# Optimization experiments

Hardware: AMD Instinct MI355X
Metric: run time of the kernel (lower is better)

## Reference

```python
import jax, jax.numpy as jnp
import numpy as np

N = 8192          # num nodes
E = 262144        # num edges
F_IN = 512        # dataset.num_features
HID = 256         # hidden_dim
C = 16            # dataset.num_classes
ALPHA = 1.0
GAMMA = 1.0
EPS = 0.4
LN_EPS = 1e-5


def setup_inputs() -> dict:
    key = jax.random.key(0)
    ks = jax.random.split(key, 16)
    x = jax.random.normal(ks[0], (N, F_IN), dtype=jnp.float32)
    edge_index = jax.random.randint(ks[1], (2, E), 0, N, dtype=jnp.int64)
    def lin(k, fan_in, fan_out):
        s = 1.0 / np.sqrt(fan_in)
        return jax.random.uniform(k, (fan_in, fan_out), jnp.float32, -s, s)
    return {
        "x": x,
        "edge_index": edge_index,
        "W0": lin(ks[2], F_IN, HID), "b0": jnp.zeros((HID,), jnp.float32),
        "ln0_g": jnp.ones((HID,), jnp.float32), "ln0_b": jnp.zeros((HID,), jnp.float32),
        "W1": lin(ks[3], HID, HID), "b1": jnp.zeros((HID,), jnp.float32),
        "ln1_g": jnp.ones((HID,), jnp.float32), "ln1_b": jnp.zeros((HID,), jnp.float32),
        "W2": lin(ks[4], HID, C), "b2": jnp.zeros((C,), jnp.float32),
    }


def _layernorm(h, g, b):
    mu = jnp.mean(h, axis=-1, keepdims=True)
    var = jnp.var(h, axis=-1, keepdims=True)
    return (h - mu) * jax.lax.rsqrt(var + LN_EPS) * g + b


def _hpf_weight_matrix(edge_index, n, dtype):
    # to_dense_adj with parallel-edge accumulation
    A = jnp.zeros((n, n), dtype).at[edge_index[0], edge_index[1]].add(jnp.asarray(1.0, dtype))
    eye = jnp.eye(n, dtype=dtype)
    A = GAMMA * A + ALPHA * eye
    # D^{-1/2} A D^{-1/2} as fused row/col scaling (same math as the two diag matmuls)
    dinv = jax.lax.rsqrt(jnp.sum(A, axis=1))
    A_hat = dinv[:, None] * A * dinv[None, :]
    # (eps - 1) I + (I - A_hat) == eps*I - A_hat ; keep only positive entries (edge extraction)
    U = EPS * eye - A_hat
    return jnp.where(U > 0, U, jnp.asarray(0.0, dtype))


def reference(x, edge_index, W0, b0, ln0_g, ln0_b, W1, b1, ln1_g, ln1_b, W2, b2):
    Wmat = _hpf_weight_matrix(edge_index, x.shape[0], x.dtype)
    # GCNConv(normalize=False): h' = scatter_{src->tgt}(w * (h@W)[src]) + bias == Wmat^T @ (h@W) + b
    def gcn(h, W, b):
        return Wmat.T @ (h @ W) + b
    h = gcn(x, W0, b0)
    h = _layernorm(jax.nn.relu(h), ln0_g, ln0_b)   # dropout p=0.0 -> identity
    h = gcn(h, W1, b1)
    h = _layernorm(jax.nn.relu(h), ln1_g, ln1_b)
    embedding = gcn(h, W2, b2)
    return embedding, jax.nn.log_softmax(embedding, axis=1)
```

## Files before the change

### kernel.cpp

```cpp
#include <hip/hip_runtime.h>

#define NN 8192
#define NE 262144
#define FIN 512
#define HIDN 256
#define NC 16

typedef __attribute__((ext_vector_type(8))) short bf16x8;
typedef __attribute__((ext_vector_type(4))) short bf16x4;
typedef __attribute__((ext_vector_type(4))) float f32x4;

static __device__ __forceinline__ unsigned short f2bf(float f) {
    union { float f; unsigned u; } v; v.f = f;
    unsigned r = v.u + 0x7FFFu + ((v.u >> 16) & 1u);
    return (unsigned short)(r >> 16);
}

template<int K, int N>
static __device__ __forceinline__ void pack_w(const float* __restrict__ W,
                                              unsigned short* __restrict__ Wp, int f) {
    constexpr int KC = K / 32;
    int lane = f & 63;
    int g = f >> 6;
    int kc = g % KC;
    int nt = g / KC;
    int n = nt * 16 + (lane & 15);
    int kbase = kc * 32 + (lane >> 4) * 8;
    bf16x8 v;
#pragma unroll
    for (int j = 0; j < 8; ++j) v[j] = (short)f2bf(W[(kbase + j) * N + n]);
    *(bf16x8*)&Wp[f * 8] = v;
}

__global__ __launch_bounds__(512) void work_kernel(
    const int* __restrict__ ei,
    const float* __restrict__ W0, const float* __restrict__ W1, const float* __restrict__ W2,
    int* __restrict__ cnt,
    unsigned short* __restrict__ Wp0, unsigned short* __restrict__ Wp1,
    unsigned short* __restrict__ Wp2)
{
    const int tid = threadIdx.x, bid = blockIdx.x;
    if (bid < 207) {
        const int p = bid * 512 + tid;
#pragma unroll
        for (int i = 0; i < 2; ++i) {
            int c = p + i * 105984;
            if (c < NE / 2) {
                int2 s2 = *(const int2*)&ei[c * 2];
                int2 t2 = *(const int2*)&ei[NE + c * 2];
                atomicAdd(&cnt[s2.x], 1);
                atomicAdd(&cnt[s2.y], 1);
                if (s2.x == t2.x) atomicAdd(&cnt[NN + s2.x], 1);
                if (s2.y == t2.y) atomicAdd(&cnt[NN + s2.y], 1);
            }
        }
    } else {
        int gp = (bid - 207) * 512 + tid;
        if (gp < 16384)       pack_w<512, 256>(W0, Wp0, gp);
        else if (gp < 24576)  pack_w<256, 256>(W1, Wp1, gp - 16384);
        else                  pack_w<256, 16 >(W2, Wp2, gp - 24576);
    }
}

static __device__ __forceinline__ void ln_epilogue(
    const f32x4 acc[2], const float* __restrict__ bias, const float* __restrict__ gam,
    const float* __restrict__ bet, const float wdr[4],
    int w, int quad, int l16,
    unsigned short* sH, float red[][16])
{
    float bv[2], gv[2], btv[2];
#pragma unroll
    for (int nt = 0; nt < 2; ++nt) {
        int col = w * 32 + nt * 16 + l16;
        bv[nt] = bias[col]; gv[nt] = gam[col]; btv[nt] = bet[col];
    }
    float vv[2][4], s[4], ss[4];
#pragma unroll
    for (int reg = 0; reg < 4; ++reg) {
        float ps = 0.f, pss = 0.f;
#pragma unroll
        for (int nt = 0; nt < 2; ++nt) {
            float v = fmaxf(fmaf(wdr[reg], acc[nt][reg], bv[nt]), 0.f);
            vv[nt][reg] = v;
            ps += v; pss += v * v;
        }
        s[reg] = ps; ss[reg] = pss;
    }
#pragma unroll
    for (int off = 1; off < 16; off <<= 1)
#pragma unroll
        for (int reg = 0; reg < 4; ++reg) {
            s[reg]  += __shfl_xor(s[reg],  off, 64);
            ss[reg] += __shfl_xor(ss[reg], off, 64);
        }
    __syncthreads();
    if (l16 == 0) {
#pragma unroll
        for (int reg = 0; reg < 4; ++reg) {
            int rl = quad * 4 + reg;
            red[rl][w * 2]     = s[reg];
            red[rl][w * 2 + 1] = ss[reg];
        }
    }
    __syncthreads();
#pragma unroll
    for (int reg = 0; reg < 4; ++reg) {
        int rl = quad * 4 + reg;
        float ts = 0.f, tss = 0.f;
#pragma unroll
        for (int i = 0; i < 8; ++i) { ts += red[rl][2 * i]; tss += red[rl][2 * i + 1]; }
        float mu  = ts * (1.0f / 256.0f);
        float var = tss * (1.0f / 256.0f) - mu * mu;
        float rs  = rsqrtf(var + 1e-5f);
#pragma unroll
        for (int nt = 0; nt < 2; ++nt) {
            float o = (vv[nt][reg] - mu) * rs * gv[nt] + btv[nt];
            sH[rl * 264 + w * 32 + nt * 16 + l16] = f2bf(o);
        }
    }
    __syncthreads();
}

__global__ __launch_bounds__(512) void mega_kernel(
    const float* __restrict__ x,
    const unsigned short* __restrict__ Wp0, const unsigned short* __restrict__ Wp1,
    const unsigned short* __restrict__ Wp2,
    const float* __restrict__ b0, const float* __restrict__ g0, const float* __restrict__ be0,
    const float* __restrict__ b1, const float* __restrict__ g1, const float* __restrict__ be1,
    const float* __restrict__ b2, const int* __restrict__ cnt,
    float* __restrict__ out)
{
    __shared__ unsigned short sX[16 * 520];
    __shared__ unsigned short sH[16 * 264];
    __shared__ float red[16][16];
    __shared__ float swd[16];

    const int tid  = threadIdx.x;
    const int lane = tid & 63, w = tid >> 6;
    const int quad = lane >> 4, l16 = lane & 15;
    const int row0 = blockIdx.x * 16;

    const float4* x4 = (const float4*)x;
    const int idx0 = tid * 2;
    float4 v0 = x4[row0 * 128 + idx0];
    float4 v1 = x4[row0 * 128 + idx0 + 1];
    float4 v2 = x4[row0 * 128 + 1024 + idx0];
    float4 v3 = x4[row0 * 128 + 1024 + idx0 + 1];

    if (tid < 16) {
        int base = cnt[2 * NN];
        int d  = cnt[row0 + tid]      - base;
        int sl = cnt[NN + row0 + tid] - base;
        float u = 0.4f - (1.0f + (float)sl) / (1.0f + (float)d);
        swd[tid] = u > 0.0f ? u : 0.0f;
    }

    {
        int r = idx0 >> 7, c4 = idx0 & 127;
        bf16x8 h;
        h[0] = (short)f2bf(v0.x); h[1] = (short)f2bf(v0.y);
        h[2] = (short)f2bf(v0.z); h[3] = (short)f2bf(v0.w);
        h[4] = (short)f2bf(v1.x); h[5] = (short)f2bf(v1.y);
        h[6] = (short)f2bf(v1.z); h[7] = (short)f2bf(v1.w);
        *(bf16x8*)&sX[r * 520 + c4 * 4] = h;
        int idx1 = idx0 + 1024;
        r = idx1 >> 7; c4 = idx1 & 127;
        h[0] = (short)f2bf(v2.x); h[1] = (short)f2bf(v2.y);
        h[2] = (short)f2bf(v2.z); h[3] = (short)f2bf(v2.w);
        h[4] = (short)f2bf(v3.x); h[5] = (short)f2bf(v3.y);
        h[6] = (short)f2bf(v3.z); h[7] = (short)f2bf(v3.w);
        *(bf16x8*)&sX[r * 520 + c4 * 4] = h;
    }
    __syncthreads();

    float wdr[4];
#pragma unroll
    for (int reg = 0; reg < 4; ++reg) wdr[reg] = swd[quad * 4 + reg];

    const bf16x8* Wp0v = (const bf16x8*)Wp0;
    const bf16x8* Wp1v = (const bf16x8*)Wp1;
    const bf16x8* Wp2v = (const bf16x8*)Wp2;

    f32x4 acc[2];
#pragma unroll
    for (int nt = 0; nt < 2; ++nt) acc[nt] = (f32x4){0.f, 0.f, 0.f, 0.f};
#pragma unroll
    for (int kc = 0; kc < 16; ++kc) {
        bf16x8 a = *(const bf16x8*)&sX[l16 * 520 + kc * 32 + quad * 8];
#pragma unroll
        for (int nt = 0; nt < 2; ++nt) {
            bf16x8 b = Wp0v[((w * 2 + nt) * 16 + kc) * 64 + lane];
            acc[nt] = __builtin_amdgcn_mfma_f32_16x16x32_bf16(a, b, acc[nt], 0, 0, 0);
        }
    }
    ln_epilogue(acc, b0, g0, be0, wdr, w, quad, l16, sH, red);

    f32x4 acc1[2];
#pragma unroll
    for (int nt = 0; nt < 2; ++nt) acc1[nt] = (f32x4){0.f, 0.f, 0.f, 0.f};
#pragma unroll
    for (int kc = 0; kc < 8; ++kc) {
        bf16x8 a = *(const bf16x8*)&sH[l16 * 264 + kc * 32 + quad * 8];
#pragma unroll
        for (int nt = 0; nt < 2; ++nt) {
            bf16x8 b = Wp1v[((w * 2 + nt) * 8 + kc) * 64 + lane];
            acc1[nt] = __builtin_amdgcn_mfma_f32_16x16x32_bf16(a, b, acc1[nt], 0, 0, 0);
        }
    }
    ln_epilogue(acc1, b1, g1, be1, wdr, w, quad, l16, sH, red);

    if (w == 0) {
        f32x4 acch = (f32x4){0.f, 0.f, 0.f, 0.f};
#pragma unroll
        for (int kc = 0; kc < 8; ++kc) {
            bf16x8 a = *(const bf16x8*)&sH[l16 * 264 + kc * 32 + quad * 8];
            bf16x8 b = Wp2v[kc * 64 + lane];
            acch = __builtin_amdgcn_mfma_f32_16x16x32_bf16(a, b, acch, 0, 0, 0);
        }
        float bb = b2[l16];
#pragma unroll
        for (int reg = 0; reg < 4; ++reg) {
            int row = row0 + quad * 4 + reg;
            float v = fmaf(wdr[reg], acch[reg], bb);
            float m = v;
#pragma unroll
            for (int off = 8; off >= 1; off >>= 1) m = fmaxf(m, __shfl_xor(m, off, 64));
            float e = __expf(v - m);
            float se = e;
#pragma unroll
            for (int off = 8; off >= 1; off >>= 1) se += __shfl_xor(se, off, 64);
            float lsm = (v - m) - __logf(se);
            out[row * 16 + l16] = v;
            out[NN * 16 + row * 16 + l16] = lsm;
        }
    }
}

extern "C" void kernel_launch(void* const* d_in, const int* in_sizes, int n_in,
                              void* d_out, int out_size, void* d_ws, size_t ws_size,
                              hipStream_t stream) {
    const float* x  = (const float*)d_in[0];
    const int*   ei = (const int*)d_in[1];
    const float* W0 = (const float*)d_in[2];
    const float* b0 = (const float*)d_in[3];
    const float* g0 = (const float*)d_in[4];
    const float* be0 = (const float*)d_in[5];
    const float* W1 = (const float*)d_in[6];
    const float* b1 = (const float*)d_in[7];
    const float* g1 = (const float*)d_in[8];
    const float* be1 = (const float*)d_in[9];
    const float* W2 = (const float*)d_in[10];
    const float* b2 = (const float*)d_in[11];
    float* out = (float*)d_out;

    char* ws = (char*)d_ws;
    int*            cnt = (int*)ws;
    unsigned short* Wp0 = (unsigned short*)(ws + 68 * 1024);
    unsigned short* Wp1 = (unsigned short*)(ws + 324 * 1024);
    unsigned short* Wp2 = (unsigned short*)(ws + 452 * 1024);

    work_kernel<<<256, 512, 0, stream>>>(ei, W0, W1, W2, cnt, Wp0, Wp1, Wp2);
    mega_kernel<<<NN / 16, 512, 0, stream>>>(x, Wp0, Wp1, Wp2,
                                             b0, g0, be0, b1, g1, be1, b2, cnt, out);
}
```

Baseline: 109.0 us.

## Replace global degree atomics with per-block LDS histograms and partial reduction

Source-degree counting moves from global atomics on 8192 counters to per-block shared-memory histograms across 48 blocks. Each block writes its histogram as a partial array, and mega_kernel sums the 48 partials per row when it computes edge weights. Edge loads widen to int4 to match. Self-loop counts still use global atomics. This cuts global atomic contention, at the cost of 1.5MB of partial writes, an extra strided reduction in the consumer, and fewer edge blocks running in parallel.

```diff
diff --git a/kernel.cpp b/kernel.cpp
--- a/kernel.cpp
+++ b/kernel.cpp
@@ -5,6 +5,7 @@
 #define FIN 512
 #define HIDN 256
 #define NC 16
+#define NHB 48
 
 typedef __attribute__((ext_vector_type(8))) short bf16x8;
 typedef __attribute__((ext_vector_type(4))) short bf16x4;
@@ -35,27 +36,41 @@
 __global__ __launch_bounds__(512) void work_kernel(
     const int* __restrict__ ei,
     const float* __restrict__ W0, const float* __restrict__ W1, const float* __restrict__ W2,
-    int* __restrict__ cnt,
+    int* __restrict__ cnt, int* __restrict__ partial,
     unsigned short* __restrict__ Wp0, unsigned short* __restrict__ Wp1,
     unsigned short* __restrict__ Wp2)
 {
+    __shared__ int hist[NN];
     const int tid = threadIdx.x, bid = blockIdx.x;
-    if (bid < 207) {
+    if (bid < NHB) {
+#pragma unroll
+        for (int i = 0; i < NN / 512; ++i) hist[tid + i * 512] = 0;
+        __syncthreads();
+        const int4* s4 = (const int4*)ei;
+        const int4* t4 = (const int4*)(ei + NE);
         const int p = bid * 512 + tid;
 #pragma unroll
-        for (int i = 0; i < 2; ++i) {
-            int c = p + i * 105984;
-            if (c < NE / 2) {
-                int2 s2 = *(const int2*)&ei[c * 2];
-                int2 t2 = *(const int2*)&ei[NE + c * 2];
-                atomicAdd(&cnt[s2.x], 1);
-                atomicAdd(&cnt[s2.y], 1);
-                if (s2.x == t2.x) atomicAdd(&cnt[NN + s2.x], 1);
-                if (s2.y == t2.y) atomicAdd(&cnt[NN + s2.y], 1);
+        for (int i = 0; i < 3; ++i) {
+            int c = p + i * (NHB * 512);
+            if (c < NE / 4) {
+                int4 s = s4[c];
+                int4 t = t4[c];
+                atomicAdd(&hist[s.x], 1);
+                atomicAdd(&hist[s.y], 1);
+                atomicAdd(&hist[s.z], 1);
+                atomicAdd(&hist[s.w], 1);
+                if (s.x == t.x) atomicAdd(&cnt[NN + s.x], 1);
+                if (s.y == t.y) atomicAdd(&cnt[NN + s.y], 1);
+                if (s.z == t.z) atomicAdd(&cnt[NN + s.z], 1);
+                if (s.w == t.w) atomicAdd(&cnt[NN + s.w], 1);
             }
         }
+        __syncthreads();
+#pragma unroll
+        for (int i = 0; i < NN / 512; ++i)
+            partial[bid * NN + tid + i * 512] = hist[tid + i * 512];
     } else {
-        int gp = (bid - 207) * 512 + tid;
+        int gp = (bid - NHB) * 512 + tid;
         if (gp < 16384)       pack_w<512, 256>(W0, Wp0, gp);
         else if (gp < 24576)  pack_w<256, 256>(W1, Wp1, gp - 16384);
         else                  pack_w<256, 16 >(W2, Wp2, gp - 24576);
@@ -128,6 +143,7 @@
     const float* __restrict__ b0, const float* __restrict__ g0, const float* __restrict__ be0,
     const float* __restrict__ b1, const float* __restrict__ g1, const float* __restrict__ be1,
     const float* __restrict__ b2, const int* __restrict__ cnt,
+    const int* __restrict__ partial,
     float* __restrict__ out)
 {
     __shared__ unsigned short sX[16 * 520];
@@ -148,8 +164,10 @@
     float4 v3 = x4[row0 * 128 + 1024 + idx0 + 1];
 
     if (tid < 16) {
+        int d = 0;
+#pragma unroll
+        for (int b = 0; b < NHB; ++b) d += partial[b * NN + row0 + tid];
         int base = cnt[2 * NN];
-        int d  = cnt[row0 + tid]      - base;
         int sl = cnt[NN + row0 + tid] - base;
         float u = 0.4f - (1.0f + (float)sl) / (1.0f + (float)d);
         swd[tid] = u > 0.0f ? u : 0.0f;
@@ -258,8 +276,9 @@
     unsigned short* Wp0 = (unsigned short*)(ws + 68 * 1024);
     unsigned short* Wp1 = (unsigned short*)(ws + 324 * 1024);
     unsigned short* Wp2 = (unsigned short*)(ws + 452 * 1024);
-
-    work_kernel<<<256, 512, 0, stream>>>(ei, W0, W1, W2, cnt, Wp0, Wp1, Wp2);
+    int*        partial = (int*)(ws + 460 * 1024);
+
+    work_kernel<<<NHB + 49, 512, 0, stream>>>(ei, W0, W1, W2, cnt, partial, Wp0, Wp1, Wp2);
     mega_kernel<<<NN / 16, 512, 0, stream>>>(x, Wp0, Wp1, Wp2,
-                                             b0, g0, be0, b1, g1, be1, b2, cnt, out);
-}
+                                             b0, g0, be0, b1, g1, be1, b2, cnt, partial, out);
+}
```

After: 101.9 us. 1.07x faster.
